# Kernel tuning notes

Measured on AMD Instinct MI355X. Metric: run time of the kernel, lower is better.

Reference implementation:

```python
import jax, jax.numpy as jnp
import numpy as np

EPS = 1e-5  # BatchNorm eps (torch default)

def _wq(w):
    # W8A16 fake-quant: per-output-channel symmetric int8 quantize + dequantize
    s = jnp.max(jnp.abs(w), axis=tuple(range(1, w.ndim)), keepdims=True) / 127.0
    s = jnp.maximum(s, 1e-8)
    q = jnp.clip(jnp.round(w / s), -128.0, 127.0)
    return q * s

def _conv(x, w, b, pad):
    y = jax.lax.conv_general_dilated(x, _wq(w), (1, 1), [(pad, pad), (pad, pad)],
                                     dimension_numbers=('NCHW', 'OIHW', 'NCHW'))
    return y + b[None, :, None, None]

def _bn(x, g, b, m, v):
    sh = (1, -1, 1, 1) if x.ndim == 4 else (1, -1)
    inv = jax.lax.rsqrt(v + EPS)
    return (x - m.reshape(sh)) * (inv * g).reshape(sh) + b.reshape(sh)

def _pool(x):
    return jax.lax.reduce_window(x, -jnp.inf, jax.lax.max, (1, 1, 2, 2), (1, 1, 2, 2), 'VALID')

def _ht(x):
    return jnp.clip(x, -1.0, 1.0)

def _linear(x, w, b):
    return x @ _wq(w).T + b

def setup_inputs() -> dict:
    key = jax.random.key(0)
    ks = iter(jax.random.split(key, 64))
    def rn(shape, s=0.05):
        return jax.random.normal(next(ks), shape, jnp.float32) * s
    d = {}
    d['x'] = jax.random.normal(next(ks), (1024, 1, 28, 28), jnp.float32)
    convs = [(1, 32, 5), (32, 64, 5), (64, 128, 3), (128, 256, 3), (256, 256, 1)]
    for i, (ci, co, k) in enumerate(convs, 1):
        d[f'w{i}'] = rn((co, ci, k, k), 0.1)
        d[f'b{i}'] = rn((co,))
        d[f'g{i}'] = jnp.ones((co,), jnp.float32)
        d[f'be{i}'] = jnp.zeros((co,), jnp.float32)
        d[f'mu{i}'] = rn((co,))
        d[f'va{i}'] = jax.random.uniform(next(ks), (co,), jnp.float32, 0.5, 1.5)
    fcs = [(2304, 1024), (1024, 512)]
    for i, (fi, fo) in enumerate(fcs, 1):
        d[f'fw{i}'] = rn((fo, fi), 0.05)
        d[f'fb{i}'] = rn((fo,))
        d[f'fg{i}'] = jnp.ones((fo,), jnp.float32)
        d[f'fbe{i}'] = jnp.zeros((fo,), jnp.float32)
        d[f'fmu{i}'] = rn((fo,))
        d[f'fva{i}'] = jax.random.uniform(next(ks), (fo,), jnp.float32, 0.5, 1.5)
    d['fw3'] = rn((10, 512), 0.05)
    d['fb3'] = rn((10,))
    return d

def reference(x, w1, b1, g1, be1, mu1, va1, w2, b2, g2, be2, mu2, va2,
              w3, b3, g3, be3, mu3, va3, w4, b4, g4, be4, mu4, va4,
              w5, b5, g5, be5, mu5, va5,
              fw1, fb1, fg1, fbe1, fmu1, fva1,
              fw2, fb2, fg2, fbe2, fmu2, fva2, fw3, fb3):
    h = _ht(_bn(_conv(x, w1, b1, 2), g1, be1, mu1, va1))                 # [B,32,28,28]
    h = _ht(_bn(_pool(_conv(h, w2, b2, 2)), g2, be2, mu2, va2))          # [B,64,14,14]
    h = _ht(_bn(_pool(_conv(h, w3, b3, 1)), g3, be3, mu3, va3))          # [B,128,7,7]
    h = _ht(_bn(_pool(_conv(h, w4, b4, 1)), g4, be4, mu4, va4))          # [B,256,3,3]
    h = _ht(_bn(_conv(h, w5, b5, 0), g5, be5, mu5, va5))                 # [B,256,3,3]
    h = h.reshape(h.shape[0], -1)                                        # [B,2304]
    h = _ht(_bn(_linear(h, fw1, fb1), fg1, fbe1, fmu1, fva1))            # [B,1024]
    h = _ht(_bn(_linear(h, fw2, fb2), fg2, fbe2, fmu2, fva2))            # [B,512]
    return _linear(h, fw3, fb3)                                          # [B,10]
```

## Files before the change

kernel.cpp:

```cpp
#include <hip/hip_runtime.h>
#include <hip/hip_bf16.h>
#include <math.h>


#define EPS 1e-5f

typedef __attribute__((ext_vector_type(8))) short bf16x8;
typedef __attribute__((ext_vector_type(4))) float f32x4;
typedef __attribute__((ext_vector_type(16))) float f32x16;
typedef __attribute__((ext_vector_type(4))) int i32x4;

__device__ __forceinline__ short f2bf(float f) {
  unsigned u = __builtin_bit_cast(unsigned, f);
  unsigned r = u + 0x7FFFu + ((u >> 16) & 1u);
  return (short)(r >> 16);
}
__device__ __forceinline__ float bf2f(short h) {
  unsigned u = ((unsigned)(unsigned short)h) << 16;
  return __builtin_bit_cast(float, u);
}
__device__ __forceinline__ int swz2(int pin) {
  return (pin ^ (pin >> 2) ^ (pin >> 5)) & 3;
}
__device__ __forceinline__ int swz3(int pin) {
  return (pin ^ (pin >> 2) ^ (pin >> 4)) & 7;
}
__device__ __forceinline__ float qclip(float w, float s) {
  return fminf(fmaxf(rintf(w / s), -128.f), 127.f);
}

struct PrepArgs {
  const float* w[8];
  short* dsth[8];
  float* dstf;
  float* sc;
  int sco[8];
  int cik[8];
  int kind[8];
  int KK[8];
  int CI[8];
  int OCCH[8];
  int KC[8];
  int cum[9];
};

__global__ __launch_bounds__(256) void prep_all(PrepArgs a) {
  int b = blockIdx.x;
  int t = 0;
  while (b >= a.cum[t + 1]) t++;
  int oc = b - a.cum[t];
  int cik = a.cik[t];
  const float* src = a.w[t] + (size_t)oc * cik;
  float m = 0.f;
  for (int i = threadIdx.x; i < cik; i += 256) m = fmaxf(m, fabsf(src[i]));
  #pragma unroll
  for (int o = 1; o < 64; o <<= 1) m = fmaxf(m, __shfl_xor(m, o));
  __shared__ float red[4];
  __shared__ float ssh;
  if ((threadIdx.x & 63) == 0) red[threadIdx.x >> 6] = m;
  __syncthreads();
  if (threadIdx.x == 0) {
    m = fmaxf(fmaxf(red[0], red[1]), fmaxf(red[2], red[3]));
    float s = fmaxf(m / 127.0f, 1e-8f);
    ssh = s;
    a.sc[a.sco[t] + oc] = s;
  }
  __syncthreads();
  const float s = ssh;
  const int kind = a.kind[t];
  short* dst = a.dsth[t];
  if (kind == 0) {
    for (int tt = threadIdx.x; tt < 32; tt += 256) {
      float q = (tt < 25) ? qclip(src[tt], s) : 0.f;
      dst[(((oc >> 4) * 4 + (tt >> 3)) * 16 + (oc & 15)) * 8 + (tt & 7)] = f2bf(q);
    }
  } else if (kind == 1) {
    const int KK = a.KK[t], CI = a.CI[t], OCCH = a.OCCH[t];
    const int NT32 = OCCH >> 5, KS16 = CI >> 4;
    const int chunk = oc / OCCH, ocl = oc - chunk * OCCH;
    const int nt = ocl >> 5, n32 = ocl & 31;
    for (int idx = threadIdx.x; idx < cik; idx += 256) {
      int ci = idx / KK, kk = idx - ci * KK;
      float q = qclip(src[idx], s);
      int ks = ci >> 4, hh = (ci >> 3) & 1, j = ci & 7;
      size_t d = ((((size_t)(chunk * KK + kk) * NT32 + nt) * KS16 + ks) * 64 +
                  hh * 32 + n32) * 8 + j;
      dst[d] = f2bf(q);
    }
  } else if (kind == 2) {
    const int KK = a.KK[t], CI = a.CI[t], OCCH = a.OCCH[t];
    const int NTC = OCCH >> 4, KS = CI >> 5;
    const int chunk = oc / OCCH, ocl = oc - chunk * OCCH;
    const int ntl = ocl >> 4, mr = ocl & 15;
    for (int idx = threadIdx.x; idx < cik; idx += 256) {
      int ci = idx / KK, kk = idx - ci * KK;
      float q = qclip(src[idx], s);
      int ks = ci >> 5, qq = (ci >> 3) & 3, j = ci & 7;
      size_t d = ((((((size_t)(chunk * KK + kk) * NTC + ntl) * KS + ks) * 4 + qq) *
                   16 + mr)) * 8 + j;
      dst[d] = f2bf(q);
    }
  } else if (kind == 3) {
    const int KC = a.KC[t];
    const int nblk = oc >> 6, ntl = (oc >> 4) & 3, mr = oc & 15;
    for (int k = threadIdx.x; k < cik; k += 256) {
      float q = qclip(src[k], s);
      size_t d = ((((((size_t)nblk * KC + (k >> 7)) * 4 + ntl) * 4 + ((k >> 5) & 3)) *
                   4 + ((k >> 3) & 3)) * 16 + mr) * 8 + (k & 7);
      dst[d] = f2bf(q);
    }
  } else {
    for (int k = threadIdx.x; k < cik; k += 256)
      a.dstf[(size_t)oc * cik + k] = qclip(src[k], s) * s;
  }
}

struct BnArgs {
  const float* p[7][5];
  const float* wsc;
  float* ab;
  int C[7];
  int abo[7];
  int sco[7];
  int cum[8];
};

__global__ __launch_bounds__(256) void bn_all(BnArgs a) {
  int i = blockIdx.x * 256 + threadIdx.x;
  if (i >= a.cum[7]) return;
  int t = 0;
  while (i >= a.cum[t + 1]) t++;
  int c = i - a.cum[t];
  float A = a.p[t][1][c] / sqrtf(a.p[t][4][c] + EPS);
  float B = (a.p[t][0][c] - a.p[t][3][c]) * A + a.p[t][2][c];
  a.ab[a.abo[t] + c] = A * a.wsc[a.sco[t] + c];
  a.ab[a.abo[t] + a.C[t] + c] = B;
}

__global__ __launch_bounds__(448, 2) void conv1_mfma(
    const float* __restrict__ x, const short* __restrict__ wb1,
    const float* __restrict__ ab, short* __restrict__ out) {
  __shared__ __align__(16) float spad[1024];
  __shared__ __align__(16) short sim[784 * 32];
  __shared__ __align__(16) short sw1[1024];
  const int tid = threadIdx.x;
  const int img = blockIdx.x;
  for (int i = tid; i < 1024; i += 448) spad[i] = 0.f;
  for (int i = tid; i < 1024; i += 448) sw1[i] = wb1[i];
  __syncthreads();
  for (int i = tid; i < 784; i += 448)
    spad[(i / 28 + 2) * 32 + (i % 28) + 2] = x[(size_t)img * 784 + i];
  __syncthreads();
  for (int p = tid; p < 784; p += 448) {
    const int py = p / 28, px = p - py * 28;
    const float* sp = &spad[py * 32 + px];
    short v[32];
    #pragma unroll
    for (int ty = 0; ty < 5; ++ty)
      #pragma unroll
      for (int tx = 0; tx < 5; ++tx)
        v[ty * 5 + tx] = f2bf(sp[ty * 32 + tx]);
    #pragma unroll
    for (int j = 25; j < 32; ++j) v[j] = 0;
    #pragma unroll
    for (int j = 0; j < 4; ++j)
      *(bf16x8*)&sim[p * 32 + j * 8] = *(const bf16x8*)&v[j * 8];
  }
  __syncthreads();
  const int lane = tid & 63, wv = tid >> 6;
  const int mrow = lane & 15, quad = lane >> 4;
  f32x4 acc[7][2];
  #pragma unroll
  for (int i = 0; i < 7; ++i) {
    acc[i][0] = (f32x4){0.f, 0.f, 0.f, 0.f};
    acc[i][1] = (f32x4){0.f, 0.f, 0.f, 0.f};
  }
  #pragma unroll
  for (int i = 0; i < 7; ++i) {
    const int mt = wv * 7 + i;
    const bf16x8 a = *(const bf16x8*)&sim[(mt * 16 + mrow) * 32 + quad * 8];
    #pragma unroll
    for (int nt = 0; nt < 2; ++nt) {
      const bf16x8 b = *(const bf16x8*)&sw1[(nt * 4 + quad) * 128 + mrow * 8];
      acc[i][nt] = __builtin_amdgcn_mfma_f32_16x16x32_bf16(a, b, acc[i][nt], 0, 0, 0);
    }
  }
  #pragma unroll
  for (int i = 0; i < 7; ++i) {
    const int mt = wv * 7 + i;
    #pragma unroll
    for (int nt = 0; nt < 2; ++nt) {
      const int oc = nt * 16 + mrow;
      const float A = ab[oc], Bc = ab[32 + oc];
      #pragma unroll
      for (int r = 0; r < 4; ++r) {
        const int p = mt * 16 + quad * 4 + r;
        float v = fminf(fmaxf(acc[i][nt][r] * A + Bc, -1.f), 1.f);
        out[((size_t)img * 784 + p) * 32 + oc] = f2bf(v);
      }
    }
  }
}

__global__ __launch_bounds__(256, 2) void conv2_half(
    const short* __restrict__ in, const short* __restrict__ wfrag,
    const float* __restrict__ ab, short* __restrict__ out) {
  constexpr int S = 4;
  constexpr int RS = 32;
  __shared__ __align__(16) short simg[18 * 32 * 32];
  __shared__ __align__(16) short sw[2][10240];
  const int tid = threadIdx.x;
  const int img = blockIdx.x >> 1, half = blockIdx.x & 1;
  const int lane = tid & 63, wv = tid >> 6;
  const int l31 = lane & 31, h = lane >> 5;

  {
    const int padrow0 = half ? 16 : 0;
    const int vrow0 = half ? 0 : 2;
    for (int c = tid; c < 512; c += 256) {
      int hp = c >> 2, blk = c & 3;
      int pin;
      if (hp < 64) {
        pin = (padrow0 + (hp >> 5)) * RS + (hp & 31);
      } else {
        int r = (hp - 64) >> 2, cc = (hp - 64) & 3;
        int col = (cc < 2) ? cc : (28 + cc);
        pin = (vrow0 + r) * RS + col;
      }
      ((i32x4*)simg)[pin * S + blk] = (i32x4){0, 0, 0, 0};
    }
  }
  {
    const i32x4* gin = (const i32x4*)(in + ((size_t)img * 784 + half * 12 * 28) * 32);
    const int vrow0 = half ? 0 : 2;
    for (int c = tid; c < 1792; c += 256) {
      int ps = c >> 2, blk = c & 3;
      int pin = (vrow0 + ps / 28) * RS + ps % 28 + 2;
      ((i32x4*)simg)[pin * S + (blk ^ swz2(pin))] = gin[c];
    }
  }

  int pinb[4], ppb[4];
  bool uv2[4];
  #pragma unroll
  for (int i = 0; i < 4; ++i) {
    int u = wv + i * 4;
    uv2[i] = u < 13;
    int m = u * 32 + l31;
    int ppl = m >> 2, cd = m & 3;
    bool ok = uv2[i] && (ppl < 98);
    int pr = ppl / 14, pc = ppl - pr * 14;
    int ygl = (half * 7 + pr) * 2 + (cd >> 1);
    int yll = ygl - (half * 14 - 2);
    int xc = pc * 2 + (cd & 1) + 2;
    pinb[i] = ok ? (yll * RS + xc) : (2 * RS + 2);
    ppb[i] = u * 8;
  }

  f32x16 acc[4][2];
  #pragma unroll
  for (int i = 0; i < 4; ++i)
    #pragma unroll
    for (int nt = 0; nt < 2; ++nt)
      #pragma unroll
      for (int e = 0; e < 16; ++e) acc[i][nt][e] = 0.f;

  i32x4 wreg[5];
  {
    const i32x4* ws0 = (const i32x4*)wfrag;
    #pragma unroll
    for (int u2 = 0; u2 < 5; ++u2) wreg[u2] = ws0[tid + u2 * 256];
    #pragma unroll
    for (int u2 = 0; u2 < 5; ++u2) ((i32x4*)sw[0])[tid + u2 * 256] = wreg[u2];
  }

  for (int tg = 0; tg < 5; ++tg) {
    __syncthreads();
    if (tg < 4) {
      const i32x4* ws = (const i32x4*)(wfrag + (size_t)(tg + 1) * 10240);
      #pragma unroll
      for (int u2 = 0; u2 < 5; ++u2) wreg[u2] = ws[tid + u2 * 256];
    }
    const short* swb = sw[tg & 1];
    const int dy = tg - 2;
    #pragma unroll
    for (int tt = 0; tt < 5; ++tt) {
      const int tp = dy * RS + (tt - 2);
      int pin[4], sx4[4];
      #pragma unroll
      for (int i = 0; i < 4; ++i) {
        pin[i] = pinb[i] + tp;
        sx4[i] = swz2(pin[i]);
      }
      #pragma unroll
      for (int ks = 0; ks < 2; ++ks) {
        bf16x8 af[4];
        #pragma unroll
        for (int i = 0; i < 4; ++i)
          af[i] = *(const bf16x8*)&simg[pin[i] * 32 + (((ks * 2 + h) ^ sx4[i]) * 8)];
        #pragma unroll
        for (int nt = 0; nt < 2; ++nt) {
          const bf16x8 bf = *(const bf16x8*)&swb[(((tt * 2 + nt) * 2 + ks) * 64 + lane) * 8];
          #pragma unroll
          for (int i = 0; i < 4; ++i)
            acc[i][nt] = __builtin_amdgcn_mfma_f32_32x32x16_bf16(af[i], bf, acc[i][nt], 0, 0, 0);
        }
      }
    }
    if (tg < 4) {
      #pragma unroll
      for (int u2 = 0; u2 < 5; ++u2)
        ((i32x4*)sw[(tg + 1) & 1])[tid + u2 * 256] = wreg[u2];
    }
  }

  #pragma unroll
  for (int i = 0; i < 4; ++i) {
    #pragma unroll
    for (int nt = 0; nt < 2; ++nt) {
      const int oc = nt * 32 + l31;
      const float A = ab[oc], Bc = ab[64 + oc];
      #pragma unroll
      for (int g = 0; g < 4; ++g) {
        const int ppo = ppb[i] + 2 * g + h;
        if (uv2[i] && ppo < 98) {
          float mx = fmaxf(fmaxf(acc[i][nt][g * 4 + 0], acc[i][nt][g * 4 + 1]),
                           fmaxf(acc[i][nt][g * 4 + 2], acc[i][nt][g * 4 + 3]));
          float v = fminf(fmaxf(mx * A + Bc, -1.f), 1.f);
          out[((size_t)img * 196 + half * 98 + ppo) * 64 + oc] = f2bf(v);
        }
      }
    }
  }
}

__global__ __launch_bounds__(256, 2) void conv3_pad(
    const short* __restrict__ in, const short* __restrict__ wfrag,
    const float* __restrict__ ab, short* __restrict__ out) {
  constexpr int S = 8, RS = 16;
  __shared__ __align__(16) short simg[2 * 256 * 64];
  __shared__ __align__(16) short sw[2][4096];
  const int tid = threadIdx.x;
  const int img0 = blockIdx.x * 2;
  const int lane = tid & 63, wv = tid >> 6;
  const int l31 = lane & 31, h = lane >> 5;

  for (int c = tid; c < 960; c += 256) {
    int blk = c & 7, hp0 = c >> 3;
    int il = hp0 >= 60 ? 1 : 0, hp = hp0 - il * 60;
    int pin;
    if (hp < 32) pin = (hp >> 4) * 15 * RS + (hp & 15);
    else {
      int r = ((hp - 32) >> 1) + 1, cc = ((hp - 32) & 1) * 15;
      pin = r * RS + cc;
    }
    ((i32x4*)simg)[(il * 256 + pin) * S + blk] = (i32x4){0, 0, 0, 0};
  }
  {
    const i32x4* gin = (const i32x4*)(in + (size_t)img0 * 196 * 64);
    for (int c = tid; c < 3136; c += 256) {
      int il = c / 1568, r = c - il * 1568;
      int ps = r >> 3, blk = r & 7;
      int pin = (ps / 14 + 1) * RS + ps % 14 + 1;
      ((i32x4*)simg)[(il * 256 + pin) * S + (blk ^ swz3(pin))] = gin[c];
    }
  }

  int pinb[4], ppb[4], ilv[4];
  bool uv4[4];
  #pragma unroll
  for (int i = 0; i < 4; ++i) {
    int u = wv + i * 4;
    uv4[i] = u < 14;
    int uu = uv4[i] ? u : 0;
    int il = uu / 7, lt = uu - il * 7;
    int m = lt * 32 + l31, ppl = m >> 2, cd = m & 3;
    bool ok = uv4[i] && (ppl < 49);
    int py = ppl / 7, px = ppl - py * 7;
    int y = py * 2 + (cd >> 1), x = px * 2 + (cd & 1);
    pinb[i] = (ok ? ((y + 1) * RS + x + 1) : (RS + 1)) + il * 256;
    ilv[i] = il;
    ppb[i] = lt * 8;
  }

  f32x16 acc[4][2];
  #pragma unroll
  for (int i = 0; i < 4; ++i)
    #pragma unroll
    for (int nt = 0; nt < 2; ++nt)
      #pragma unroll
      for (int e = 0; e < 16; ++e) acc[i][nt][e] = 0.f;

  i32x4 wreg[2];
  {
    const i32x4* ws0 = (const i32x4*)wfrag;
    wreg[0] = ws0[tid];
    wreg[1] = ws0[tid + 256];
    ((i32x4*)sw[0])[tid] = wreg[0];
    ((i32x4*)sw[0])[tid + 256] = wreg[1];
  }

  for (int s = 0; s < 18; ++s) {
    __syncthreads();
    if (s < 17) {
      const i32x4* ws = (const i32x4*)(wfrag + (size_t)(s + 1) * 4096);
      wreg[0] = ws[tid];
      wreg[1] = ws[tid + 256];
    }
    const short* swb = sw[s & 1];
    const int t = s % 9;
    const int tp = (t / 3 - 1) * RS + (t % 3 - 1);
    int pin[4], sx4[4];
    #pragma unroll
    for (int i = 0; i < 4; ++i) {
      pin[i] = pinb[i] + tp;
      sx4[i] = swz3(pin[i]);
    }
    #pragma unroll
    for (int ks = 0; ks < 4; ++ks) {
      bf16x8 af[4];
      #pragma unroll
      for (int i = 0; i < 4; ++i)
        af[i] = *(const bf16x8*)&simg[pin[i] * 64 + (((ks * 2 + h) ^ sx4[i]) * 8)];
      #pragma unroll
      for (int nt = 0; nt < 2; ++nt) {
        const bf16x8 bf = *(const bf16x8*)&swb[((nt * 4 + ks) * 64 + lane) * 8];
        #pragma unroll
        for (int i = 0; i < 4; ++i)
          acc[i][nt] = __builtin_amdgcn_mfma_f32_32x32x16_bf16(af[i], bf, acc[i][nt], 0, 0, 0);
      }
    }
    if (s < 17) {
      ((i32x4*)sw[(s + 1) & 1])[tid] = wreg[0];
      ((i32x4*)sw[(s + 1) & 1])[tid + 256] = wreg[1];
    }
    if (t == 8) {
      const int ch = s / 9;
      #pragma unroll
      for (int i = 0; i < 4; ++i) {
        #pragma unroll
        for (int nt = 0; nt < 2; ++nt) {
          const int oc = ch * 64 + nt * 32 + l31;
          const float A = ab[oc], Bc = ab[128 + oc];
          #pragma unroll
          for (int g = 0; g < 4; ++g) {
            const int ppo = ppb[i] + 2 * g + h;
            if (uv4[i] && ppo < 49) {
              float mx = fmaxf(fmaxf(acc[i][nt][g * 4 + 0], acc[i][nt][g * 4 + 1]),
                               fmaxf(acc[i][nt][g * 4 + 2], acc[i][nt][g * 4 + 3]));
              float v = fminf(fmaxf(mx * A + Bc, -1.f), 1.f);
              out[((size_t)(img0 + ilv[i]) * 49 + ppo) * 128 + oc] = f2bf(v);
            }
          }
          #pragma unroll
          for (int e = 0; e < 16; ++e) acc[i][nt][e] = 0.f;
        }
      }
    }
  }
}

__global__ __launch_bounds__(512, 2) void conv4_mfma(
    const short* __restrict__ in,
    const short* __restrict__ wfrag,
    const float* __restrict__ ab,
    short* __restrict__ outH, short* __restrict__ outL) {
  constexpr int S = 16, NPIX = 49, PP = 9;
  __shared__ __align__(16) short simg[2 * NPIX * 128];
  __shared__ __align__(16) short swb[2][32768];
  const int tid = threadIdx.x;
  const int img0 = blockIdx.x * 2;
  const int lane = tid & 63, wv = tid >> 6;
  const int mrow = lane & 15, quad = lane >> 4;

  {
    const i32x4* gsrc = (const i32x4*)(in + (size_t)img0 * NPIX * 128);
    for (int c = tid; c < 2 * NPIX * S; c += 512) {
      int il = c / (NPIX * S);
      int r = c - il * (NPIX * S);
      int pix = r >> 4, blk = r & 15;
      ((i32x4*)simg)[il * NPIX * S + pix * S + (blk ^ (pix & 15))] = gsrc[c];
    }
    for (int u = tid; u < 4096; u += 512)
      ((i32x4*)swb[0])[u] = ((const i32x4*)wfrag)[u];
  }

  int yy[6], xx[6], ibs[6], ppo_[6], ilv[6];
  bool rv[6], pv[6];
  #pragma unroll
  for (int i = 0; i < 6; ++i) {
    int il = i / 3, lt = i - il * 3;
    int m = lt * 16 + mrow;
    int pp = m >> 2, cd = m & 3;
    rv[i] = pp < PP;
    int py = pp / 3, px = pp - py * 3;
    yy[i] = py * 2 + (cd >> 1);
    xx[i] = px * 2 + (cd & 1);
    ibs[i] = il * NPIX * S;
    ilv[i] = il;
    ppo_[i] = lt * 4 + quad;
    pv[i] = ppo_[i] < PP;
  }
  const int nt0 = wv, nt1 = wv + 8;
  f32x4 acc[6][2];
  #pragma unroll
  for (int i = 0; i < 6; ++i) {
    acc[i][0] = (f32x4){0.f, 0.f, 0.f, 0.f};
    acc[i][1] = (f32x4){0.f, 0.f, 0.f, 0.f};
  }
  __syncthreads();

  int dy = -1, dx = -1;
  for (int t = 0; t < 9; ++t) {
    const int buf = t & 1;
    if (t < 8) {
      const i32x4* wsrc = (const i32x4*)(wfrag + (size_t)(t + 1) * 32768);
      for (int u = tid; u < 4096; u += 512) ((i32x4*)swb[buf ^ 1])[u] = wsrc[u];
    }
    #pragma unroll
    for (int ks = 0; ks < 4; ++ks) {
      bf16x8 af[6];
      #pragma unroll
      for (int i = 0; i < 6; ++i) {
        int iy = yy[i] + dy, ix = xx[i] + dx;
        bool ok = rv[i] && (unsigned)iy < 7u && (unsigned)ix < 7u;
        int pin = iy * 7 + ix;
        int blk = (ks * 4 + quad) ^ (pin & 15);
        af[i] = ok ? *(const bf16x8*)&simg[(ibs[i] + pin * S + blk) * 8]
                   : (bf16x8){0, 0, 0, 0, 0, 0, 0, 0};
      }
      const bf16x8 b0 = *(const bf16x8*)&swb[buf][((nt0 * 4 + ks) * 4 + quad) * 128 + mrow * 8];
      const bf16x8 b1 = *(const bf16x8*)&swb[buf][((nt1 * 4 + ks) * 4 + quad) * 128 + mrow * 8];
      #pragma unroll
      for (int i = 0; i < 6; ++i) {
        acc[i][0] = __builtin_amdgcn_mfma_f32_16x16x32_bf16(af[i], b0, acc[i][0], 0, 0, 0);
        acc[i][1] = __builtin_amdgcn_mfma_f32_16x16x32_bf16(af[i], b1, acc[i][1], 0, 0, 0);
      }
    }
    dx++;
    if (dx == 2) { dx = -1; dy++; }
    __syncthreads();
  }

  #pragma unroll
  for (int i = 0; i < 6; ++i) {
    if (pv[i]) {
      #pragma unroll
      for (int nj = 0; nj < 2; ++nj) {
        const int oc = (nj ? nt1 : nt0) * 16 + mrow;
        const f32x4 a = acc[i][nj];
        float mx = fmaxf(fmaxf(a[0], a[1]), fmaxf(a[2], a[3]));
        float v = fminf(fmaxf(mx * ab[oc] + ab[256 + oc], -1.f), 1.f);
        const int m5 = (img0 + ilv[i]) * 9 + ppo_[i];
        size_t d = ((((((size_t)(m5 >> 6) * 2 + (oc >> 7)) * 4 + ((m5 >> 4) & 3)) * 4 +
                     ((oc >> 5) & 3)) * 4 + ((oc >> 3) & 3)) * 16 + (m5 & 15)) * 8 + (oc & 7);
        short hi = f2bf(v);
        outH[d] = hi;
        outL[d] = f2bf(v - bf2f(hi));
      }
    }
  }
}

template <int KC, int OUTMODE, int KC2, int NALL>
__global__ __launch_bounds__(256, 2) void fc_mfma(
    const short* __restrict__ Xh, const short* __restrict__ Xl,
    const short* __restrict__ Wf, const float* __restrict__ ab,
    float* __restrict__ outF, short* __restrict__ outH, short* __restrict__ outL) {
  __shared__ __align__(16) short swt[2][8192];
  const int tid = threadIdx.x;
  const int bn = blockIdx.x, bm = blockIdx.y;
  const int lane = tid & 63, wv = tid >> 6;
  const int mrow = lane & 15, quad = lane >> 4;
  f32x4 acc[4];
  #pragma unroll
  for (int nt = 0; nt < 4; ++nt) acc[nt] = (f32x4){0.f, 0.f, 0.f, 0.f};

  i32x4 wreg[4];
  {
    const i32x4* ws0 = (const i32x4*)(Wf + (size_t)bn * KC * 8192);
    #pragma unroll
    for (int u = 0; u < 4; ++u) wreg[u] = ws0[tid + u * 256];
    #pragma unroll
    for (int u = 0; u < 4; ++u) ((i32x4*)swt[0])[tid + u * 256] = wreg[u];
  }

  for (int kc = 0; kc < KC; ++kc) {
    __syncthreads();
    if (kc < KC - 1) {
      const i32x4* ws = (const i32x4*)(Wf + ((size_t)bn * KC + kc + 1) * 8192);
      #pragma unroll
      for (int u = 0; u < 4; ++u) wreg[u] = ws[tid + u * 256];
    }
    const short* xb = Xh + (((size_t)bm * KC + kc) * 4 + wv) * 2048;
    const short* xlb = Xl + (((size_t)bm * KC + kc) * 4 + wv) * 2048;
    const short* swb = swt[kc & 1];
    #pragma unroll
    for (int ks = 0; ks < 4; ++ks) {
      const int ao = ((ks * 4 + quad) * 16 + mrow) * 8;
      const bf16x8 ah = *(const bf16x8*)&xb[ao];
      const bf16x8 al = *(const bf16x8*)&xlb[ao];
      #pragma unroll
      for (int nt = 0; nt < 4; ++nt) {
        const bf16x8 b = *(const bf16x8*)&swb[(((nt * 4 + ks) * 4 + quad) * 16 + mrow) * 8];
        acc[nt] = __builtin_amdgcn_mfma_f32_16x16x32_bf16(ah, b, acc[nt], 0, 0, 0);
        acc[nt] = __builtin_amdgcn_mfma_f32_16x16x32_bf16(al, b, acc[nt], 0, 0, 0);
      }
    }
    if (kc < KC - 1) {
      #pragma unroll
      for (int u = 0; u < 4; ++u)
        ((i32x4*)swt[(kc + 1) & 1])[tid + u * 256] = wreg[u];
    }
  }

  #pragma unroll
  for (int nt = 0; nt < 4; ++nt) {
    const int n = bn * 64 + nt * 16 + mrow;
    const float A = ab[n], Bc = ab[NALL + n];
    #pragma unroll
    for (int r = 0; r < 4; ++r) {
      const int m = bm * 64 + wv * 16 + quad * 4 + r;
      float v = fminf(fmaxf(acc[nt][r] * A + Bc, -1.f), 1.f);
      if (OUTMODE == 0) {
        size_t d = (((((((size_t)(m >> 6) * KC2 + (n >> 7)) * 4 + ((m >> 4) & 3)) * 4 +
                       ((n >> 5) & 3)) * 4 + ((n >> 3) & 3)) * 16 + (m & 15))) * 8 + (n & 7);
        short hi = f2bf(v);
        outH[d] = hi;
        outL[d] = f2bf(v - bf2f(hi));
      } else if (OUTMODE == 1) {
        outF[(size_t)m * NALL + n] = v;
      } else {
        const int imgq = m / 9, p = m - imgq * 9;
        const int k1 = n * 9 + p;
        size_t d = ((((((size_t)(imgq >> 6) * KC2 + (k1 >> 7)) * 4 + ((imgq >> 4) & 3)) * 4 +
                     ((k1 >> 5) & 3)) * 4 + ((k1 >> 3) & 3)) * 16 + (imgq & 15)) * 8 + (k1 & 7);
        short hi = f2bf(v);
        outH[d] = hi;
        outL[d] = f2bf(v - bf2f(hi));
      }
    }
  }
}

__global__ __launch_bounds__(256) void fc3_kernel(
    const float* __restrict__ X, const float* __restrict__ W,
    const float* __restrict__ bias, float* __restrict__ out) {
  __shared__ float ws[512 * 10 + 16];
  for (int li = threadIdx.x; li < 5120; li += 256) {
    int n = li / 512, k = li - n * 512;
    ws[k * 10 + n] = W[li];
  }
  __syncthreads();
  const int il = threadIdx.x >> 4, n = threadIdx.x & 15;
  const int img = blockIdx.x * 16 + il;
  if (n < 10) {
    const float4* xp = (const float4*)(X + (size_t)img * 512);
    float s = 0.f;
    for (int k4 = 0; k4 < 128; ++k4) {
      const float4 xv = xp[k4];
      const int k = k4 * 4;
      s += xv.x * ws[k * 10 + n];
      s += xv.y * ws[(k + 1) * 10 + n];
      s += xv.z * ws[(k + 2) * 10 + n];
      s += xv.w * ws[(k + 3) * 10 + n];
    }
    out[img * 10 + n] = s + bias[n];
  }
}

extern "C" void kernel_launch(void* const* d_in, const int* in_sizes, int n_in,
                              void* d_out, int out_size, void* d_ws, size_t ws_size,
                              hipStream_t stream) {
  (void)in_sizes; (void)n_in; (void)out_size; (void)ws_size;
  const float* x = (const float*)d_in[0];
  float* W = (float*)d_ws;

  float* wsc  = W + 0;
  float* ab   = W + 2304;
  float* fq3  = W + 6912;
  short* wb1  = (short*)(W + 12032);
  short* wb2  = (short*)(W + 12544);
  short* wb3  = (short*)(W + 38144);
  short* wb4  = (short*)(W + 75008);
  short* wb5  = (short*)(W + 222464);
  short* fqb1 = (short*)(W + 255232);
  short* fqb2 = (short*)(W + 1434880);
  short* h1   = (short*)(W + 1697024);
  short* h2   = (short*)(W + 14542080);
  short* h3   = (short*)(W + 20964608);
  short* h4h  = (short*)(W + 24175872);
  short* h4l  = (short*)(W + 25355520);
  short* h5h  = (short*)(W + 26535168);
  short* h5l  = (short*)(W + 27714816);
  short* f1h  = (short*)(W + 28894464);
  short* f1l  = (short*)(W + 29418752);
  float* f2   = W + 29943040;

  PrepArgs pa;
  const int widx[8] = {1, 7, 13, 19, 25, 31, 37, 43};
  short* pdst[8] = {wb1, wb2, wb3, wb4, wb5, fqb1, fqb2, nullptr};
  const int sco8[8] = {0, 32, 96, 224, 480, 736, 1760, 2272};
  const int cik8[8] = {25, 800, 576, 1152, 256, 2304, 1024, 512};
  const int co8[8] = {32, 64, 128, 256, 256, 1024, 512, 10};
  const int kind8[8] = {0, 1, 1, 2, 3, 3, 3, 4};
  const int KK8[8] = {25, 25, 9, 9, 1, 1, 1, 1};
  const int CI8[8] = {1, 32, 64, 128, 256, 2304, 1024, 512};
  const int OCCH8[8] = {32, 64, 64, 256, 256, 1024, 512, 10};
  const int KC8[8] = {1, 1, 1, 1, 2, 18, 8, 1};
  int cum = 0;
  for (int i = 0; i < 8; ++i) {
    pa.w[i] = (const float*)d_in[widx[i]];
    pa.dsth[i] = pdst[i];
    pa.sco[i] = sco8[i];
    pa.cik[i] = cik8[i];
    pa.kind[i] = kind8[i];
    pa.KK[i] = KK8[i];
    pa.CI[i] = CI8[i];
    pa.OCCH[i] = OCCH8[i];
    pa.KC[i] = KC8[i];
    pa.cum[i] = cum;
    cum += co8[i];
  }
  pa.cum[8] = cum;
  pa.dstf = fq3;
  pa.sc = wsc;
  hipLaunchKernelGGL(prep_all, dim3(cum), dim3(256), 0, stream, pa);

  BnArgs ba;
  const int bbase[7] = {2, 8, 14, 20, 26, 32, 38};
  const int bc[7] = {32, 64, 128, 256, 256, 1024, 512};
  const int abo[7] = {0, 64, 192, 448, 960, 1472, 3520};
  int bcum = 0;
  for (int t = 0; t < 7; ++t) {
    for (int j = 0; j < 5; ++j) ba.p[t][j] = (const float*)d_in[bbase[t] + j];
    ba.C[t] = bc[t];
    ba.abo[t] = abo[t];
    ba.sco[t] = sco8[t];
    ba.cum[t] = bcum;
    bcum += bc[t];
  }
  ba.cum[7] = bcum;
  ba.ab = ab;
  ba.wsc = wsc;
  hipLaunchKernelGGL(bn_all, dim3((bcum + 255) / 256), dim3(256), 0, stream, ba);

  hipLaunchKernelGGL(conv1_mfma, dim3(1024), dim3(448), 0, stream,
                     x, wb1, ab + 0, h1);
  hipLaunchKernelGGL(conv2_half, dim3(2048), dim3(256), 0, stream,
                     h1, wb2, ab + 64, h2);
  hipLaunchKernelGGL(conv3_pad, dim3(512), dim3(256), 0, stream,
                     h2, wb3, ab + 192, h3);
  hipLaunchKernelGGL(conv4_mfma, dim3(512), dim3(512), 0, stream,
                     h3, wb4, ab + 448, h4h, h4l);
  hipLaunchKernelGGL((fc_mfma<2, 2, 18, 256>), dim3(4, 144), dim3(256), 0, stream,
                     h4h, h4l, wb5, ab + 960, nullptr, h5h, h5l);

  hipLaunchKernelGGL((fc_mfma<18, 0, 8, 1024>), dim3(16, 16), dim3(256), 0, stream,
                     h5h, h5l, fqb1, ab + 1472, nullptr, f1h, f1l);
  hipLaunchKernelGGL((fc_mfma<8, 1, 0, 512>), dim3(8, 16), dim3(256), 0, stream,
                     f1h, f1l, fqb2, ab + 3520, f2, nullptr, nullptr);
  hipLaunchKernelGGL(fc3_kernel, dim3(64), dim3(256), 0, stream,
                     f2, fq3, (const float*)d_in[44], (float*)d_out);
}
```

Baseline: 422.3 us.

## Read conv and FC weight fragments directly from global memory instead of LDS staging

Removes the double-buffered LDS staging of weight fragments in conv2, conv3, conv4 and the FC kernel, so MFMA B operands are loaded straight from global memory (L1/L2 cached) and the per-tap __syncthreads barriers disappear. The conv loops are fully unrolled over taps, and the FC kernel's launch bound is raised to 4 blocks per SM since it no longer uses shared memory. This cuts LDS traffic, LDS footprint and barrier stalls, but exposes global-load latency on every weight fragment read and relies on cache hits across waves.

New measurement: 608.1 us. 44.0% more time.

```diff
diff --git a/kernel.cpp b/kernel.cpp
--- a/kernel.cpp
+++ b/kernel.cpp
@@ -208,7 +208,6 @@
   constexpr int S = 4;
   constexpr int RS = 32;
   __shared__ __align__(16) short simg[18 * 32 * 32];
-  __shared__ __align__(16) short sw[2][10240];
   const int tid = threadIdx.x;
   const int img = blockIdx.x >> 1, half = blockIdx.x & 1;
   const int lane = tid & 63, wv = tid >> 6;
@@ -265,52 +264,30 @@
       #pragma unroll
       for (int e = 0; e < 16; ++e) acc[i][nt][e] = 0.f;
 
-  i32x4 wreg[5];
-  {
-    const i32x4* ws0 = (const i32x4*)wfrag;
-    #pragma unroll
-    for (int u2 = 0; u2 < 5; ++u2) wreg[u2] = ws0[tid + u2 * 256];
-    #pragma unroll
-    for (int u2 = 0; u2 < 5; ++u2) ((i32x4*)sw[0])[tid + u2 * 256] = wreg[u2];
-  }
-
-  for (int tg = 0; tg < 5; ++tg) {
-    __syncthreads();
-    if (tg < 4) {
-      const i32x4* ws = (const i32x4*)(wfrag + (size_t)(tg + 1) * 10240);
-      #pragma unroll
-      for (int u2 = 0; u2 < 5; ++u2) wreg[u2] = ws[tid + u2 * 256];
-    }
-    const short* swb = sw[tg & 1];
-    const int dy = tg - 2;
-    #pragma unroll
-    for (int tt = 0; tt < 5; ++tt) {
-      const int tp = dy * RS + (tt - 2);
-      int pin[4], sx4[4];
-      #pragma unroll
-      for (int i = 0; i < 4; ++i) {
-        pin[i] = pinb[i] + tp;
-        sx4[i] = swz2(pin[i]);
-      }
-      #pragma unroll
-      for (int ks = 0; ks < 2; ++ks) {
-        bf16x8 af[4];
+  __syncthreads();
+
+  #pragma unroll
+  for (int t = 0; t < 25; ++t) {
+    const int tp = (t / 5 - 2) * RS + (t % 5 - 2);
+    int pin[4], sx4[4];
+    #pragma unroll
+    for (int i = 0; i < 4; ++i) {
+      pin[i] = pinb[i] + tp;
+      sx4[i] = swz2(pin[i]);
+    }
+    #pragma unroll
+    for (int ks = 0; ks < 2; ++ks) {
+      bf16x8 af[4];
+      #pragma unroll
+      for (int i = 0; i < 4; ++i)
+        af[i] = *(const bf16x8*)&simg[pin[i] * 32 + (((ks * 2 + h) ^ sx4[i]) * 8)];
+      #pragma unroll
+      for (int nt = 0; nt < 2; ++nt) {
+        const bf16x8 bf = *(const bf16x8*)&wfrag[(((t * 2 + nt) * 2 + ks) * 64 + lane) * 8];
         #pragma unroll
         for (int i = 0; i < 4; ++i)
-          af[i] = *(const bf16x8*)&simg[pin[i] * 32 + (((ks * 2 + h) ^ sx4[i]) * 8)];
-        #pragma unroll
-        for (int nt = 0; nt < 2; ++nt) {
-          const bf16x8 bf = *(const bf16x8*)&swb[(((tt * 2 + nt) * 2 + ks) * 64 + lane) * 8];
-          #pragma unroll
-          for (int i = 0; i < 4; ++i)
-            acc[i][nt] = __builtin_amdgcn_mfma_f32_32x32x16_bf16(af[i], bf, acc[i][nt], 0, 0, 0);
-        }
-      }
-    }
-    if (tg < 4) {
-      #pragma unroll
-      for (int u2 = 0; u2 < 5; ++u2)
-        ((i32x4*)sw[(tg + 1) & 1])[tid + u2 * 256] = wreg[u2];
+          acc[i][nt] = __builtin_amdgcn_mfma_f32_32x32x16_bf16(af[i], bf, acc[i][nt], 0, 0, 0);
+      }
     }
   }
 
@@ -339,7 +316,6 @@
     const float* __restrict__ ab, short* __restrict__ out) {
   constexpr int S = 8, RS = 16;
   __shared__ __align__(16) short simg[2 * 256 * 64];
-  __shared__ __align__(16) short sw[2][4096];
   const int tid = threadIdx.x;
   const int img0 = blockIdx.x * 2;
   const int lane = tid & 63, wv = tid >> 6;
@@ -391,70 +367,52 @@
       #pragma unroll
       for (int e = 0; e < 16; ++e) acc[i][nt][e] = 0.f;
 
-  i32x4 wreg[2];
-  {
-    const i32x4* ws0 = (const i32x4*)wfrag;
-    wreg[0] = ws0[tid];
-    wreg[1] = ws0[tid + 256];
-    ((i32x4*)sw[0])[tid] = wreg[0];
-    ((i32x4*)sw[0])[tid + 256] = wreg[1];
-  }
-
-  for (int s = 0; s < 18; ++s) {
-    __syncthreads();
-    if (s < 17) {
-      const i32x4* ws = (const i32x4*)(wfrag + (size_t)(s + 1) * 4096);
-      wreg[0] = ws[tid];
-      wreg[1] = ws[tid + 256];
-    }
-    const short* swb = sw[s & 1];
-    const int t = s % 9;
-    const int tp = (t / 3 - 1) * RS + (t % 3 - 1);
-    int pin[4], sx4[4];
-    #pragma unroll
-    for (int i = 0; i < 4; ++i) {
-      pin[i] = pinb[i] + tp;
-      sx4[i] = swz3(pin[i]);
-    }
-    #pragma unroll
-    for (int ks = 0; ks < 4; ++ks) {
-      bf16x8 af[4];
-      #pragma unroll
-      for (int i = 0; i < 4; ++i)
-        af[i] = *(const bf16x8*)&simg[pin[i] * 64 + (((ks * 2 + h) ^ sx4[i]) * 8)];
-      #pragma unroll
-      for (int nt = 0; nt < 2; ++nt) {
-        const bf16x8 bf = *(const bf16x8*)&swb[((nt * 4 + ks) * 64 + lane) * 8];
+  __syncthreads();
+
+  for (int ch = 0; ch < 2; ++ch) {
+    #pragma unroll
+    for (int t = 0; t < 9; ++t) {
+      const int tp = (t / 3 - 1) * RS + (t % 3 - 1);
+      int pin[4], sx4[4];
+      #pragma unroll
+      for (int i = 0; i < 4; ++i) {
+        pin[i] = pinb[i] + tp;
+        sx4[i] = swz3(pin[i]);
+      }
+      #pragma unroll
+      for (int ks = 0; ks < 4; ++ks) {
+        bf16x8 af[4];
         #pragma unroll
         for (int i = 0; i < 4; ++i)
-          acc[i][nt] = __builtin_amdgcn_mfma_f32_32x32x16_bf16(af[i], bf, acc[i][nt], 0, 0, 0);
-      }
-    }
-    if (s < 17) {
-      ((i32x4*)sw[(s + 1) & 1])[tid] = wreg[0];
-      ((i32x4*)sw[(s + 1) & 1])[tid + 256] = wreg[1];
-    }
-    if (t == 8) {
-      const int ch = s / 9;
-      #pragma unroll
-      for (int i = 0; i < 4; ++i) {
+          af[i] = *(const bf16x8*)&simg[pin[i] * 64 + (((ks * 2 + h) ^ sx4[i]) * 8)];
         #pragma unroll
         for (int nt = 0; nt < 2; ++nt) {
-          const int oc = ch * 64 + nt * 32 + l31;
-          const float A = ab[oc], Bc = ab[128 + oc];
+          const bf16x8 bf = *(const bf16x8*)&wfrag[
+              ((((ch * 9 + t) * 2 + nt) * 4 + ks) * 64 + lane) * 8];
           #pragma unroll
-          for (int g = 0; g < 4; ++g) {
-            const int ppo = ppb[i] + 2 * g + h;
-            if (uv4[i] && ppo < 49) {
-              float mx = fmaxf(fmaxf(acc[i][nt][g * 4 + 0], acc[i][nt][g * 4 + 1]),
-                               fmaxf(acc[i][nt][g * 4 + 2], acc[i][nt][g * 4 + 3]));
-              float v = fminf(fmaxf(mx * A + Bc, -1.f), 1.f);
-              out[((size_t)(img0 + ilv[i]) * 49 + ppo) * 128 + oc] = f2bf(v);
-            }
+          for (int i = 0; i < 4; ++i)
+            acc[i][nt] = __builtin_amdgcn_mfma_f32_32x32x16_bf16(af[i], bf, acc[i][nt], 0, 0, 0);
+        }
+      }
+    }
+    #pragma unroll
+    for (int i = 0; i < 4; ++i) {
+      #pragma unroll
+      for (int nt = 0; nt < 2; ++nt) {
+        const int oc = ch * 64 + nt * 32 + l31;
+        const float A = ab[oc], Bc = ab[128 + oc];
+        #pragma unroll
+        for (int g = 0; g < 4; ++g) {
+          const int ppo = ppb[i] + 2 * g + h;
+          if (uv4[i] && ppo < 49) {
+            float mx = fmaxf(fmaxf(acc[i][nt][g * 4 + 0], acc[i][nt][g * 4 + 1]),
+                             fmaxf(acc[i][nt][g * 4 + 2], acc[i][nt][g * 4 + 3]));
+            float v = fminf(fmaxf(mx * A + Bc, -1.f), 1.f);
+            out[((size_t)(img0 + ilv[i]) * 49 + ppo) * 128 + oc] = f2bf(v);
           }
-          #pragma unroll
-          for (int e = 0; e < 16; ++e) acc[i][nt][e] = 0.f;
         }
+        #pragma unroll
+        for (int e = 0; e < 16; ++e) acc[i][nt][e] = 0.f;
       }
     }
   }
@@ -467,7 +425,6 @@
     short* __restrict__ outH, short* __restrict__ outL) {
   constexpr int S = 16, NPIX = 49, PP = 9;
   __shared__ __align__(16) short simg[2 * NPIX * 128];
-  __shared__ __align__(16) short swb[2][32768];
   const int tid = threadIdx.x;
   const int img0 = blockIdx.x * 2;
   const int lane = tid & 63, wv = tid >> 6;
@@ -481,8 +438,6 @@
       int pix = r >> 4, blk = r & 15;
       ((i32x4*)simg)[il * NPIX * S + pix * S + (blk ^ (pix & 15))] = gsrc[c];
     }
-    for (int u = tid; u < 4096; u += 512)
-      ((i32x4*)swb[0])[u] = ((const i32x4*)wfrag)[u];
   }
 
   int yy[6], xx[6], ibs[6], ppo_[6], ilv[6];
@@ -510,13 +465,9 @@
   }
   __syncthreads();
 
-  int dy = -1, dx = -1;
+  #pragma unroll
   for (int t = 0; t < 9; ++t) {
-    const int buf = t & 1;
-    if (t < 8) {
-      const i32x4* wsrc = (const i32x4*)(wfrag + (size_t)(t + 1) * 32768);
-      for (int u = tid; u < 4096; u += 512) ((i32x4*)swb[buf ^ 1])[u] = wsrc[u];
-    }
+    const int dy = t / 3 - 1, dx = t % 3 - 1;
     #pragma unroll
     for (int ks = 0; ks < 4; ++ks) {
       bf16x8 af[6];
@@ -529,17 +480,16 @@
         af[i] = ok ? *(const bf16x8*)&simg[(ibs[i] + pin * S + blk) * 8]
                    : (bf16x8){0, 0, 0, 0, 0, 0, 0, 0};
       }
-      const bf16x8 b0 = *(const bf16x8*)&swb[buf][((nt0 * 4 + ks) * 4 + quad) * 128 + mrow * 8];
-      const bf16x8 b1 = *(const bf16x8*)&swb[buf][((nt1 * 4 + ks) * 4 + quad) * 128 + mrow * 8];
+      const bf16x8 b0 = *(const bf16x8*)&wfrag[
+          (size_t)t * 32768 + ((nt0 * 4 + ks) * 4 + quad) * 128 + mrow * 8];
+      const bf16x8 b1 = *(const bf16x8*)&wfrag[
+          (size_t)t * 32768 + ((nt1 * 4 + ks) * 4 + quad) * 128 + mrow * 8];
       #pragma unroll
       for (int i = 0; i < 6; ++i) {
         acc[i][0] = __builtin_amdgcn_mfma_f32_16x16x32_bf16(af[i], b0, acc[i][0], 0, 0, 0);
         acc[i][1] = __builtin_amdgcn_mfma_f32_16x16x32_bf16(af[i], b1, acc[i][1], 0, 0, 0);
       }
     }
-    dx++;
-    if (dx == 2) { dx = -1; dy++; }
-    __syncthreads();
   }
 
   #pragma unroll
@@ -563,11 +513,10 @@
 }
 
 template <int KC, int OUTMODE, int KC2, int NALL>
-__global__ __launch_bounds__(256, 2) void fc_mfma(
+__global__ __launch_bounds__(256, 4) void fc_mfma(
     const short* __restrict__ Xh, const short* __restrict__ Xl,
     const short* __restrict__ Wf, const float* __restrict__ ab,
     float* __restrict__ outF, short* __restrict__ outH, short* __restrict__ outL) {
-  __shared__ __align__(16) short swt[2][8192];
   const int tid = threadIdx.x;
   const int bn = blockIdx.x, bm = blockIdx.y;
   const int lane = tid & 63, wv = tid >> 6;
@@ -576,25 +525,10 @@
   #pragma unroll
   for (int nt = 0; nt < 4; ++nt) acc[nt] = (f32x4){0.f, 0.f, 0.f, 0.f};
 
-  i32x4 wreg[4];
-  {
-    const i32x4* ws0 = (const i32x4*)(Wf + (size_t)bn * KC * 8192);
-    #pragma unroll
-    for (int u = 0; u < 4; ++u) wreg[u] = ws0[tid + u * 256];
-    #pragma unroll
-    for (int u = 0; u < 4; ++u) ((i32x4*)swt[0])[tid + u * 256] = wreg[u];
-  }
-
   for (int kc = 0; kc < KC; ++kc) {
-    __syncthreads();
-    if (kc < KC - 1) {
-      const i32x4* ws = (const i32x4*)(Wf + ((size_t)bn * KC + kc + 1) * 8192);
-      #pragma unroll
-      for (int u = 0; u < 4; ++u) wreg[u] = ws[tid + u * 256];
-    }
     const short* xb = Xh + (((size_t)bm * KC + kc) * 4 + wv) * 2048;
     const short* xlb = Xl + (((size_t)bm * KC + kc) * 4 + wv) * 2048;
-    const short* swb = swt[kc & 1];
+    const short* wb = Wf + ((size_t)bn * KC + kc) * 8192;
     #pragma unroll
     for (int ks = 0; ks < 4; ++ks) {
       const int ao = ((ks * 4 + quad) * 16 + mrow) * 8;
@@ -602,15 +536,10 @@
       const bf16x8 al = *(const bf16x8*)&xlb[ao];
       #pragma unroll
       for (int nt = 0; nt < 4; ++nt) {
-        const bf16x8 b = *(const bf16x8*)&swb[(((nt * 4 + ks) * 4 + quad) * 16 + mrow) * 8];
+        const bf16x8 b = *(const bf16x8*)&wb[(((nt * 4 + ks) * 4 + quad) * 16 + mrow) * 8];
         acc[nt] = __builtin_amdgcn_mfma_f32_16x16x32_bf16(ah, b, acc[nt], 0, 0, 0);
         acc[nt] = __builtin_amdgcn_mfma_f32_16x16x32_bf16(al, b, acc[nt], 0, 0, 0);
       }
-    }
-    if (kc < KC - 1) {
-      #pragma unroll
-      for (int u = 0; u < 4; ++u)
-        ((i32x4*)swt[(kc + 1) & 1])[tid + u * 256] = wreg[u];
     }
   }
 
```
